# Kernel optimization log

Hardware: AMD Instinct MI355X
Metric: run time of the kernel (lower is better)

Reference implementation:

```python
import jax, jax.numpy as jnp
import numpy as np

DIM = 1024
HEADS = 16
DIM_HEAD = 64
INNER = HEADS * DIM_HEAD  # 1024
EPS = 1e-5


def layer_norm(x, g, b):
    mu = jnp.mean(x, axis=-1, keepdims=True)
    var = jnp.var(x, axis=-1, keepdims=True)
    return (x - mu) * jax.lax.rsqrt(var + EPS) * g + b


def setup_inputs() -> dict:
    key = jax.random.key(0)
    ks = jax.random.split(key, 8)
    s = 0.02
    return {
        "x": jax.random.normal(ks[0], (2, 2048, DIM), dtype=jnp.float32),
        "w_qkv": jax.random.normal(ks[1], (DIM, 3 * INNER), dtype=jnp.float32) * s,
        "w_out": jax.random.normal(ks[2], (INNER, DIM), dtype=jnp.float32) * s,
        "b_out": jnp.zeros((DIM,), jnp.float32),
        "g1": jnp.ones((DIM,), jnp.float32),
        "bt1": jnp.zeros((DIM,), jnp.float32),
        "g2": jnp.ones((DIM,), jnp.float32),
        "bt2": jnp.zeros((DIM,), jnp.float32),
        "w1": jax.random.normal(ks[3], (DIM, DIM), dtype=jnp.float32) * s,  # ff hidden = dim_out = DIM
        "b1": jnp.zeros((DIM,), jnp.float32),
        "w2": jax.random.normal(ks[4], (DIM, DIM), dtype=jnp.float32) * s,
        "b2": jnp.zeros((DIM,), jnp.float32),
    }


def reference(x, w_qkv, w_out, b_out, g1, bt1, g2, bt2, w1, b1, w2, b2):
    b, n, _ = x.shape
    scale = DIM_HEAD ** (-0.5)
    x_in = x
    xl = layer_norm(x, g1, bt1)
    qkv = xl @ w_qkv  # [b, n, 3*inner]
    q, k, v = jnp.split(qkv, 3, axis=-1)
    def split_heads(t):
        return t.reshape(b, n, HEADS, DIM_HEAD).transpose(0, 2, 1, 3)  # b h n d
    q, k, v = map(split_heads, (q, k, v))
    dots = jnp.einsum('bhid,bhjd->bhij', q, k) * scale
    attn = jax.nn.softmax(dots, axis=-1)
    out = jnp.einsum('bhij,bhjd->bhid', attn, v)
    out = out.transpose(0, 2, 1, 3).reshape(b, n, INNER)
    out = out @ w_out + b_out
    out = out + x_in
    h = layer_norm(out, g2, bt2)
    h = jax.nn.gelu(h @ w1 + b1, approximate=False) @ w2 + b2
    return h + out
```

## Files before the change

kernel.cpp:

```cpp
#include <hip/hip_runtime.h>
#include <math.h>

typedef __attribute__((ext_vector_type(4))) float f32x4;
typedef __attribute__((ext_vector_type(8))) short bf16x8;
typedef __attribute__((ext_vector_type(8))) unsigned short u16x8;

#define DIM 1024
#define SEQ 2048
#define NHEADS 16
#define DH 64

__device__ __forceinline__ unsigned short f2bf(float f) {
    unsigned int u = __builtin_bit_cast(unsigned int, f);
    u += 0x7fffu + ((u >> 16) & 1u);
    return (unsigned short)(u >> 16);
}

__device__ __forceinline__ unsigned int cvt_pk_bf16(float lo, float hi) {
    unsigned int r;
    asm("v_cvt_pk_bf16_f32 %0, %1, %2" : "=v"(r) : "v"(lo), "v"(hi));
    return r;
}

__device__ __forceinline__ float fexp2(float x) {
    float r;
    asm("v_exp_f32 %0, %1" : "=v"(r) : "v"(x));
    return r;
}

__device__ __forceinline__ void gld16(const unsigned short* g, unsigned short* l) {
    __builtin_amdgcn_global_load_lds((const __attribute__((address_space(1))) void*)g,
                                     (__attribute__((address_space(3))) void*)l, 16, 0, 0);
}

__global__ __launch_bounds__(256) void wtrans_all(const float* __restrict__ wq,
                                                  const float* __restrict__ wo,
                                                  const float* __restrict__ wf1,
                                                  const float* __restrict__ wf2,
                                                  unsigned short* __restrict__ oq,
                                                  unsigned short* __restrict__ oo,
                                                  unsigned short* __restrict__ of1,
                                                  unsigned short* __restrict__ of2, float sc) {
    int z = blockIdx.z;
    int bxi = blockIdx.x;
    if (z > 0 && bxi >= 32) return;
    const float* w = z == 0 ? wq : z == 1 ? wo : z == 2 ? wf1 : wf2;
    unsigned short* wt = z == 0 ? oq : z == 1 ? oo : z == 2 ? of1 : of2;
    int N = z == 0 ? 3072 : 1024;
    int scale_n = z == 0 ? 1024 : 0;
    const int K = 1024;
    __shared__ float t[32][33];
    int tid = threadIdx.x;
    int n0 = bxi * 32, k0 = blockIdx.y * 32;
    int c = tid & 31, rb = tid >> 5;
#pragma unroll
    for (int i = 0; i < 4; ++i) {
        int r = rb + i * 8;
        t[r][c] = w[(size_t)(k0 + r) * N + n0 + c];
    }
    __syncthreads();
#pragma unroll
    for (int i = 0; i < 4; ++i) {
        int r = rb + i * 8;
        float v = t[c][r];
        if (n0 + r < scale_n) v *= sc;
        wt[(size_t)(n0 + r) * K + k0 + c] = f2bf(v);
    }
}

__global__ __launch_bounds__(256) void ln_kernel(const float* __restrict__ x,
                                                 const float* __restrict__ g,
                                                 const float* __restrict__ bt,
                                                 unsigned short* __restrict__ o) {
    int row = blockIdx.x, tid = threadIdx.x;
    const float4* xr = (const float4*)(x + (size_t)row * DIM);
    float4 v = xr[tid];
    float s1 = v.x + v.y + v.z + v.w;
    float s2 = v.x * v.x + v.y * v.y + v.z * v.z + v.w * v.w;
#pragma unroll
    for (int m = 32; m >= 1; m >>= 1) {
        s1 += __shfl_xor(s1, m);
        s2 += __shfl_xor(s2, m);
    }
    __shared__ float r1[4], r2[4];
    int w = tid >> 6;
    if ((tid & 63) == 0) { r1[w] = s1; r2[w] = s2; }
    __syncthreads();
    s1 = r1[0] + r1[1] + r1[2] + r1[3];
    s2 = r2[0] + r2[1] + r2[2] + r2[3];
    float mu = s1 * (1.0f / DIM);
    float var = s2 * (1.0f / DIM) - mu * mu;
    float rstd = rsqrtf(var + 1e-5f);
    float4 g4 = ((const float4*)g)[tid];
    float4 b4 = ((const float4*)bt)[tid];
    ushort4 ov;
    ov.x = f2bf((v.x - mu) * rstd * g4.x + b4.x);
    ov.y = f2bf((v.y - mu) * rstd * g4.y + b4.y);
    ov.z = f2bf((v.z - mu) * rstd * g4.z + b4.z);
    ov.w = f2bf((v.w - mu) * rstd * g4.w + b4.w);
    *(ushort4*)(o + (size_t)row * DIM + tid * 4) = ov;
}

template <int BN, int BK, int OBF, int BIAS, int GELU_, int RESID>
__global__ __launch_bounds__(256) void gemm_kernel(const unsigned short* __restrict__ A,
                                                   const unsigned short* __restrict__ BT,
                                                   void* __restrict__ C,
                                                   const float* __restrict__ bias,
                                                   const float* __restrict__ resid,
                                                   int M, int N, int K, int nbx) {
    constexpr int U = BK / 8;
    constexpr int NAU = 128 * U;
    constexpr int NBU = BN * U;
    constexpr int PT = (NAU + NBU) / 256;
    constexpr int NJ = BN / 32;
    constexpr int KK = BK / 32;
    __shared__ unsigned short As[3][128 * BK];
    __shared__ unsigned short Bs[3][BN * BK];
    int tid = threadIdx.x;
    int lane = tid & 63, w = tid >> 6;
    int l15 = lane & 15, lhi = lane >> 4;
    int nwg = gridDim.x, wg = blockIdx.x;
    int swz = (wg & 7) * (nwg >> 3) + (wg >> 3);
    int bx = swz % nbx, by = swz / nbx;
    int row0 = by * 128, col0 = bx * BN;
    int wrow = (w >> 1) * 64, wcol = (w & 1) * (16 * NJ);
    f32x4 zero = {0.f, 0.f, 0.f, 0.f};
    f32x4 acc[4][NJ];
#pragma unroll
    for (int i = 0; i < 4; ++i)
#pragma unroll
        for (int j = 0; j < NJ; ++j) acc[i][j] = zero;
    auto stage = [&](int buf, int kt) {
#pragma unroll
        for (int p = 0; p < PT; ++p) {
            if (p * 256 < NAU) {
                int u = tid + p * 256;
                int r = u / U, cu = u % U;
                int scu = cu ^ (r & (U - 1));
                gld16(A + (size_t)(row0 + r) * K + kt * BK + scu * 8, &As[buf][0] + u * 8);
            } else {
                int ub = tid + p * 256 - NAU;
                int r = ub / U, cu = ub % U;
                int scu = cu ^ (r & (U - 1));
                gld16(BT + (size_t)(col0 + r) * K + kt * BK + scu * 8, &Bs[buf][0] + ub * 8);
            }
        }
    };
    int nk = K / BK;
    stage(0, 0);
    stage(1, 1);
    asm volatile("s_waitcnt vmcnt(%0)" ::"i"(PT) : "memory");
    __builtin_amdgcn_s_barrier();
    __builtin_amdgcn_sched_barrier(0);
    int cur = 0;
    for (int kt = 0; kt < nk; ++kt) {
        int nxt2 = cur + 2 >= 3 ? cur - 1 : cur + 2;
        if (kt + 2 < nk) stage(nxt2, kt + 2);
        const unsigned short* Ab = &As[cur][0];
        const unsigned short* Bb = &Bs[cur][0];
        bf16x8 af[4][KK], bfr[NJ][KK];
#pragma unroll
        for (int i = 0; i < 4; ++i)
#pragma unroll
            for (int kk = 0; kk < KK; ++kk) {
                int rr = wrow + i * 16 + l15;
                int up = (kk * 4 + lhi) ^ (rr & (U - 1));
                af[i][kk] = *(const bf16x8*)&Ab[rr * BK + up * 8];
            }
#pragma unroll
        for (int j = 0; j < NJ; ++j)
#pragma unroll
            for (int kk = 0; kk < KK; ++kk) {
                int rr = wcol + j * 16 + l15;
                int up = (kk * 4 + lhi) ^ (rr & (U - 1));
                bfr[j][kk] = *(const bf16x8*)&Bb[rr * BK + up * 8];
            }
#pragma unroll
        for (int kk = 0; kk < KK; ++kk)
#pragma unroll
            for (int i = 0; i < 4; ++i)
#pragma unroll
                for (int j = 0; j < NJ; ++j)
                    acc[i][j] = __builtin_amdgcn_mfma_f32_16x16x32_bf16(af[i][kk], bfr[j][kk],
                                                                        acc[i][j], 0, 0, 0);
        __builtin_amdgcn_sched_barrier(0);
        if (kt + 1 < nk) {
            if (kt + 2 < nk)
                asm volatile("s_waitcnt vmcnt(%0)" ::"i"(PT) : "memory");
            else
                asm volatile("s_waitcnt vmcnt(0)" ::: "memory");
            __builtin_amdgcn_s_barrier();
            __builtin_amdgcn_sched_barrier(0);
        }
        cur = cur + 1 == 3 ? 0 : cur + 1;
    }
#pragma unroll
    for (int i = 0; i < 4; ++i)
#pragma unroll
        for (int j = 0; j < NJ; ++j)
#pragma unroll
            for (int r = 0; r < 4; ++r) {
                int row = row0 + wrow + i * 16 + lhi * 4 + r;
                int col = col0 + wcol + j * 16 + l15;
                float v = acc[i][j][r];
                if (BIAS) v += bias[col];
                if (GELU_) v = 0.5f * v * (1.0f + erff(v * 0.70710678118f));
                if (RESID) v += resid[(size_t)row * N + col];
                if (OBF)
                    ((unsigned short*)C)[(size_t)row * N + col] = f2bf(v);
                else
                    ((float*)C)[(size_t)row * N + col] = v;
            }
}

__global__ __launch_bounds__(256) void vtrans_kernel(const unsigned short* __restrict__ qkv,
                                                     unsigned short* __restrict__ vt) {
    __shared__ unsigned short t[64 * 72];
    int tid = threadIdx.x;
    int nt = blockIdx.x & 31, h = (blockIdx.x >> 5) & 15, b = blockIdx.x >> 9;
#pragma unroll
    for (int p = 0; p < 2; ++p) {
        int c = tid + p * 256;
        int n = c >> 3, s = (c & 7) * 8;
        *(uint4*)&t[n * 72 + s] =
            *(const uint4*)(qkv + (size_t)(b * SEQ + nt * 64 + n) * 3072 + 2048 + h * 64 + s);
    }
    __syncthreads();
#pragma unroll
    for (int p = 0; p < 2; ++p) {
        int c = tid + p * 256;
        int d = c >> 3, s0 = (c & 7) * 8;
        u16x8 val;
#pragma unroll
        for (int j = 0; j < 8; ++j) {
            int s = s0 + j;
            int sig = (s & 32) | ((s & 4) << 2) | ((s & 24) >> 1) | (s & 3);
            val[j] = t[sig * 72 + d];
        }
        *(u16x8*)(vt + ((size_t)(b * NHEADS + h) * DH + d) * SEQ + nt * 64 + s0) = val;
    }
}

__global__ __launch_bounds__(256) void attn_kernel(const unsigned short* __restrict__ qkv,
                                                   const unsigned short* __restrict__ vt,
                                                   unsigned short* __restrict__ o) {
    __shared__ unsigned short Ks[3][64 * 64];
    __shared__ unsigned short Vs[3][64 * 64];
    int tid = threadIdx.x;
    int lane = tid & 63, w = tid >> 6;
    int l15 = lane & 15, lhi = lane >> 4;
    int wg = blockIdx.x;
    int swz = (wg & 7) * 64 + (wg >> 3);
    int qt = swz & 15, h = (swz >> 4) & 15, b = swz >> 8;
    bf16x8 qf[2][2];
#pragma unroll
    for (int qg = 0; qg < 2; ++qg) {
        const unsigned short* qb =
            qkv + (size_t)(b * SEQ + qt * 128 + w * 32 + qg * 16 + l15) * 3072 + h * DH;
        qf[qg][0] = *(const bf16x8*)(qb + lhi * 8);
        qf[qg][1] = *(const bf16x8*)(qb + 32 + lhi * 8);
    }
    f32x4 zero = {0.f, 0.f, 0.f, 0.f};
    f32x4 oacc[2][4], lacc[2];
#pragma unroll
    for (int qg = 0; qg < 2; ++qg) {
        lacc[qg] = zero;
#pragma unroll
        for (int i = 0; i < 4; ++i) oacc[qg][i] = zero;
    }
    const short one_s = (short)0x3F80;
    bf16x8 ones = {one_s, one_s, one_s, one_s, one_s, one_s, one_s, one_s};
    int srow = tid >> 3;
    int scx = (tid & 7) ^ (srow & 7);
    const unsigned short* kb = qkv + (size_t)b * SEQ * 3072 + 1024 + h * DH;
    const unsigned short* vb = vt + (size_t)(b * NHEADS + h) * DH * SEQ;
    const unsigned short* k0 = kb + (size_t)srow * 3072 + scx * 8;
    const unsigned short* v0 = vb + (size_t)srow * SEQ + scx * 8;
    auto stage = [&](int buf, int kt) {
        unsigned short* lk = &Ks[buf][0] + tid * 8;
        unsigned short* lv = &Vs[buf][0] + tid * 8;
        gld16(k0 + (size_t)kt * 64 * 3072, lk);
        gld16(k0 + ((size_t)kt * 64 + 32) * 3072, lk + 2048);
        gld16(v0 + kt * 64, lv);
        gld16(v0 + (size_t)32 * SEQ + kt * 64, lv + 2048);
    };
    const int NT = SEQ / 64;
    stage(0, 0);
    stage(1, 1);
    asm volatile("s_waitcnt vmcnt(4)" ::: "memory");
    __builtin_amdgcn_s_barrier();
    __builtin_amdgcn_sched_barrier(0);
    int kx = l15 & 7;
    int cur = 0;
    for (int kt = 0; kt < NT; ++kt) {
        int nxt2 = cur + 2 >= 3 ? cur - 1 : cur + 2;
        if (kt + 2 < NT) stage(nxt2, kt + 2);
        const unsigned short* Kc = &Ks[cur][0];
        const unsigned short* Vc = &Vs[cur][0];
        f32x4 sacc[2][4];
#pragma unroll
        for (int nt = 0; nt < 4; ++nt) {
            bf16x8 kf0 = *(const bf16x8*)&Kc[(nt * 16 + l15) * 64 + ((lhi ^ kx) * 8)];
            bf16x8 kf1 = *(const bf16x8*)&Kc[(nt * 16 + l15) * 64 + (((4 + lhi) ^ kx) * 8)];
#pragma unroll
            for (int qg = 0; qg < 2; ++qg) {
                f32x4 z = __builtin_amdgcn_mfma_f32_16x16x32_bf16(kf0, qf[qg][0], zero, 0, 0, 0);
                sacc[qg][nt] = __builtin_amdgcn_mfma_f32_16x16x32_bf16(kf1, qf[qg][1], z, 0, 0, 0);
            }
        }
        bf16x8 pf[2][2];
#pragma unroll
        for (int qg = 0; qg < 2; ++qg)
#pragma unroll
            for (int kc = 0; kc < 2; ++kc) {
                union { bf16x8 v; unsigned int u[4]; } pu;
                pu.u[0] = cvt_pk_bf16(fexp2(sacc[qg][2 * kc][0]), fexp2(sacc[qg][2 * kc][1]));
                pu.u[1] = cvt_pk_bf16(fexp2(sacc[qg][2 * kc][2]), fexp2(sacc[qg][2 * kc][3]));
                pu.u[2] = cvt_pk_bf16(fexp2(sacc[qg][2 * kc + 1][0]), fexp2(sacc[qg][2 * kc + 1][1]));
                pu.u[3] = cvt_pk_bf16(fexp2(sacc[qg][2 * kc + 1][2]), fexp2(sacc[qg][2 * kc + 1][3]));
                pf[qg][kc] = pu.v;
            }
#pragma unroll
        for (int dt = 0; dt < 4; ++dt)
#pragma unroll
            for (int kc = 0; kc < 2; ++kc) {
                bf16x8 vf = *(const bf16x8*)&Vc[(dt * 16 + l15) * 64 + (((kc * 4 + lhi) ^ kx) * 8)];
#pragma unroll
                for (int qg = 0; qg < 2; ++qg)
                    oacc[qg][dt] =
                        __builtin_amdgcn_mfma_f32_16x16x32_bf16(vf, pf[qg][kc], oacc[qg][dt], 0, 0, 0);
            }
#pragma unroll
        for (int qg = 0; qg < 2; ++qg) {
            lacc[qg] = __builtin_amdgcn_mfma_f32_16x16x32_bf16(ones, pf[qg][0], lacc[qg], 0, 0, 0);
            lacc[qg] = __builtin_amdgcn_mfma_f32_16x16x32_bf16(ones, pf[qg][1], lacc[qg], 0, 0, 0);
        }
        __builtin_amdgcn_sched_barrier(0);
        if (kt + 1 < NT) {
            if (kt + 2 < NT)
                asm volatile("s_waitcnt vmcnt(4)" ::: "memory");
            else
                asm volatile("s_waitcnt vmcnt(0)" ::: "memory");
            __builtin_amdgcn_s_barrier();
            __builtin_amdgcn_sched_barrier(0);
        }
        cur = cur + 1 == 3 ? 0 : cur + 1;
    }
#pragma unroll
    for (int qg = 0; qg < 2; ++qg) {
        float rl = 1.0f / lacc[qg][0];
        size_t orow = (size_t)(b * SEQ + qt * 128 + w * 32 + qg * 16 + l15) * DIM + h * DH;
#pragma unroll
        for (int dt = 0; dt < 4; ++dt) {
            ushort4 st;
            st.x = f2bf(oacc[qg][dt][0] * rl);
            st.y = f2bf(oacc[qg][dt][1] * rl);
            st.z = f2bf(oacc[qg][dt][2] * rl);
            st.w = f2bf(oacc[qg][dt][3] * rl);
            *(ushort4*)(o + orow + dt * 16 + lhi * 4) = st;
        }
    }
}

extern "C" void kernel_launch(void* const* d_in, const int* in_sizes, int n_in,
                              void* d_out, int out_size, void* d_ws, size_t ws_size,
                              hipStream_t stream) {
    (void)in_sizes; (void)n_in; (void)out_size; (void)ws_size;
    const float* x = (const float*)d_in[0];
    const float* w_qkv = (const float*)d_in[1];
    const float* w_out = (const float*)d_in[2];
    const float* b_out = (const float*)d_in[3];
    const float* g1 = (const float*)d_in[4];
    const float* bt1 = (const float*)d_in[5];
    const float* g2 = (const float*)d_in[6];
    const float* bt2 = (const float*)d_in[7];
    const float* w1 = (const float*)d_in[8];
    const float* b1 = (const float*)d_in[9];
    const float* w2 = (const float*)d_in[10];
    const float* b2 = (const float*)d_in[11];
    float* out = (float*)d_out;

    char* ws = (char*)d_ws;
    size_t off = 0;
    auto alloc = [&](size_t bytes) {
        void* p = ws + off;
        off += (bytes + 255) & ~(size_t)255;
        return p;
    };
    const int R = 2 * SEQ;
    unsigned short* xl    = (unsigned short*)alloc((size_t)R * DIM * 2);
    unsigned short* wqkvT = (unsigned short*)alloc((size_t)3 * DIM * DIM * 2);
    unsigned short* woutT = (unsigned short*)alloc((size_t)DIM * DIM * 2);
    unsigned short* w1T   = (unsigned short*)alloc((size_t)DIM * DIM * 2);
    unsigned short* w2T   = (unsigned short*)alloc((size_t)DIM * DIM * 2);
    unsigned short* qkvb  = (unsigned short*)alloc((size_t)R * 3 * DIM * 2);
    unsigned short* vtb   = (unsigned short*)alloc((size_t)R * DIM * 2);
    unsigned short* attO  = (unsigned short*)alloc((size_t)R * DIM * 2);
    unsigned short* h2    = (unsigned short*)alloc((size_t)R * DIM * 2);
    unsigned short* ffn1  = (unsigned short*)alloc((size_t)R * DIM * 2);

    const float CS = 0.125f * 1.44269504f;
    wtrans_all<<<dim3(96, 32, 4), 256, 0, stream>>>(w_qkv, w_out, w1, w2, wqkvT, woutT, w1T, w2T, CS);

    ln_kernel<<<R, 256, 0, stream>>>(x, g1, bt1, xl);
    gemm_kernel<128, 32, 1, 0, 0, 0><<<dim3((3 * DIM / 128) * (R / 128)), 256, 0, stream>>>(
        xl, wqkvT, qkvb, nullptr, nullptr, R, 3 * DIM, DIM, 3 * DIM / 128);
    vtrans_kernel<<<2 * NHEADS * (SEQ / 64), 256, 0, stream>>>(qkvb, vtb);
    attn_kernel<<<2 * NHEADS * (SEQ / 128), 256, 0, stream>>>(qkvb, vtb, attO);
    gemm_kernel<64, 64, 0, 1, 0, 1><<<dim3((DIM / 64) * (R / 128)), 256, 0, stream>>>(
        attO, woutT, out, b_out, x, R, DIM, DIM, DIM / 64);
    ln_kernel<<<R, 256, 0, stream>>>(out, g2, bt2, h2);
    gemm_kernel<64, 64, 1, 1, 1, 0><<<dim3((DIM / 64) * (R / 128)), 256, 0, stream>>>(
        h2, w1T, ffn1, b1, nullptr, R, DIM, DIM, DIM / 64);
    gemm_kernel<64, 64, 0, 1, 0, 1><<<dim3((DIM / 64) * (R / 128)), 256, 0, stream>>>(
        ffn1, w2T, out, b2, out, R, DIM, DIM, DIM / 64);
}
```

Before: 170.0 us.

## Split attention over two key halves with a separate combine kernel

Splits each attention workgroup's key range into two halves, doubling the grid to 1024 blocks. Each block writes unnormalised partial outputs (bf16) and row sums, and a new combine kernel adds the halves and normalises. The triple-buffered async K/V pipeline is replaced with a single buffer that waits for each load before computing, which removes load/compute overlap. It also adds extra global traffic and a kernel launch, and rounds partial sums to bf16 before they are combined. The combine is valid because the softmax uses no running max, so the partial sums are plain sums.

```diff
diff --git a/kernel.cpp b/kernel.cpp
--- a/kernel.cpp
+++ b/kernel.cpp
@@ -14,6 +14,11 @@
     unsigned int u = __builtin_bit_cast(unsigned int, f);
     u += 0x7fffu + ((u >> 16) & 1u);
     return (unsigned short)(u >> 16);
+}
+
+__device__ __forceinline__ float bf2f(unsigned short s) {
+    unsigned int u = (unsigned int)s << 16;
+    return __builtin_bit_cast(float, u);
 }
 
 __device__ __forceinline__ unsigned int cvt_pk_bf16(float lo, float hi) {
@@ -243,15 +248,16 @@
 
 __global__ __launch_bounds__(256) void attn_kernel(const unsigned short* __restrict__ qkv,
                                                    const unsigned short* __restrict__ vt,
-                                                   unsigned short* __restrict__ o) {
-    __shared__ unsigned short Ks[3][64 * 64];
-    __shared__ unsigned short Vs[3][64 * 64];
+                                                   unsigned short* __restrict__ po,
+                                                   float* __restrict__ pl) {
+    __shared__ unsigned short Ks[64 * 64];
+    __shared__ unsigned short Vs[64 * 64];
     int tid = threadIdx.x;
     int lane = tid & 63, w = tid >> 6;
     int l15 = lane & 15, lhi = lane >> 4;
     int wg = blockIdx.x;
-    int swz = (wg & 7) * 64 + (wg >> 3);
-    int qt = swz & 15, h = (swz >> 4) & 15, b = swz >> 8;
+    int swz = (wg & 7) * 128 + (wg >> 3);
+    int qt = swz & 15, half = (swz >> 4) & 1, h = (swz >> 5) & 15, b = swz >> 9;
     bf16x8 qf[2][2];
 #pragma unroll
     for (int qg = 0; qg < 2; ++qg) {
@@ -276,32 +282,26 @@
     const unsigned short* vb = vt + (size_t)(b * NHEADS + h) * DH * SEQ;
     const unsigned short* k0 = kb + (size_t)srow * 3072 + scx * 8;
     const unsigned short* v0 = vb + (size_t)srow * SEQ + scx * 8;
-    auto stage = [&](int buf, int kt) {
-        unsigned short* lk = &Ks[buf][0] + tid * 8;
-        unsigned short* lv = &Vs[buf][0] + tid * 8;
-        gld16(k0 + (size_t)kt * 64 * 3072, lk);
-        gld16(k0 + ((size_t)kt * 64 + 32) * 3072, lk + 2048);
-        gld16(v0 + kt * 64, lv);
-        gld16(v0 + (size_t)32 * SEQ + kt * 64, lv + 2048);
+    auto stage = [&](int kg) {
+        unsigned short* lk = &Ks[0] + tid * 8;
+        unsigned short* lv = &Vs[0] + tid * 8;
+        gld16(k0 + (size_t)kg * 64 * 3072, lk);
+        gld16(k0 + ((size_t)kg * 64 + 32) * 3072, lk + 2048);
+        gld16(v0 + kg * 64, lv);
+        gld16(v0 + (size_t)32 * SEQ + kg * 64, lv + 2048);
     };
-    const int NT = SEQ / 64;
-    stage(0, 0);
-    stage(1, 1);
-    asm volatile("s_waitcnt vmcnt(4)" ::: "memory");
-    __builtin_amdgcn_s_barrier();
-    __builtin_amdgcn_sched_barrier(0);
     int kx = l15 & 7;
-    int cur = 0;
-    for (int kt = 0; kt < NT; ++kt) {
-        int nxt2 = cur + 2 >= 3 ? cur - 1 : cur + 2;
-        if (kt + 2 < NT) stage(nxt2, kt + 2);
-        const unsigned short* Kc = &Ks[cur][0];
-        const unsigned short* Vc = &Vs[cur][0];
+    const int NT2 = SEQ / 64 / 2;
+    for (int kt = 0; kt < NT2; ++kt) {
+        stage(half * NT2 + kt);
+        asm volatile("s_waitcnt vmcnt(0)" ::: "memory");
+        __builtin_amdgcn_s_barrier();
+        __builtin_amdgcn_sched_barrier(0);
         f32x4 sacc[2][4];
 #pragma unroll
         for (int nt = 0; nt < 4; ++nt) {
-            bf16x8 kf0 = *(const bf16x8*)&Kc[(nt * 16 + l15) * 64 + ((lhi ^ kx) * 8)];
-            bf16x8 kf1 = *(const bf16x8*)&Kc[(nt * 16 + l15) * 64 + (((4 + lhi) ^ kx) * 8)];
+            bf16x8 kf0 = *(const bf16x8*)&Ks[(nt * 16 + l15) * 64 + ((lhi ^ kx) * 8)];
+            bf16x8 kf1 = *(const bf16x8*)&Ks[(nt * 16 + l15) * 64 + (((4 + lhi) ^ kx) * 8)];
 #pragma unroll
             for (int qg = 0; qg < 2; ++qg) {
                 f32x4 z = __builtin_amdgcn_mfma_f32_16x16x32_bf16(kf0, qf[qg][0], zero, 0, 0, 0);
@@ -324,7 +324,7 @@
         for (int dt = 0; dt < 4; ++dt)
 #pragma unroll
             for (int kc = 0; kc < 2; ++kc) {
-                bf16x8 vf = *(const bf16x8*)&Vc[(dt * 16 + l15) * 64 + (((kc * 4 + lhi) ^ kx) * 8)];
+                bf16x8 vf = *(const bf16x8*)&Vs[(dt * 16 + l15) * 64 + (((kc * 4 + lhi) ^ kx) * 8)];
 #pragma unroll
                 for (int qg = 0; qg < 2; ++qg)
                     oacc[qg][dt] =
@@ -336,30 +336,42 @@
             lacc[qg] = __builtin_amdgcn_mfma_f32_16x16x32_bf16(ones, pf[qg][1], lacc[qg], 0, 0, 0);
         }
         __builtin_amdgcn_sched_barrier(0);
-        if (kt + 1 < NT) {
-            if (kt + 2 < NT)
-                asm volatile("s_waitcnt vmcnt(4)" ::: "memory");
-            else
-                asm volatile("s_waitcnt vmcnt(0)" ::: "memory");
+        if (kt + 1 < NT2) {
             __builtin_amdgcn_s_barrier();
             __builtin_amdgcn_sched_barrier(0);
         }
-        cur = cur + 1 == 3 ? 0 : cur + 1;
     }
 #pragma unroll
     for (int qg = 0; qg < 2; ++qg) {
-        float rl = 1.0f / lacc[qg][0];
-        size_t orow = (size_t)(b * SEQ + qt * 128 + w * 32 + qg * 16 + l15) * DIM + h * DH;
+        int rrow = b * SEQ + qt * 128 + w * 32 + qg * 16 + l15;
+        unsigned short* pob = po + ((size_t)half * 4096 + rrow) * DIM + h * DH;
 #pragma unroll
         for (int dt = 0; dt < 4; ++dt) {
             ushort4 st;
-            st.x = f2bf(oacc[qg][dt][0] * rl);
-            st.y = f2bf(oacc[qg][dt][1] * rl);
-            st.z = f2bf(oacc[qg][dt][2] * rl);
-            st.w = f2bf(oacc[qg][dt][3] * rl);
-            *(ushort4*)(o + orow + dt * 16 + lhi * 4) = st;
-        }
-    }
+            st.x = f2bf(oacc[qg][dt][0]);
+            st.y = f2bf(oacc[qg][dt][1]);
+            st.z = f2bf(oacc[qg][dt][2]);
+            st.w = f2bf(oacc[qg][dt][3]);
+            *(ushort4*)(pob + dt * 16 + lhi * 4) = st;
+        }
+        if (lhi == 0) pl[((size_t)half * 4096 + rrow) * NHEADS + h] = lacc[qg][0];
+    }
+}
+
+__global__ __launch_bounds__(256) void attn_combine(const unsigned short* __restrict__ po,
+                                                    const float* __restrict__ pl,
+                                                    unsigned short* __restrict__ o) {
+    int r = blockIdx.x, tid = threadIdx.x;
+    int d0 = tid * 4, h = d0 >> 6;
+    ushort4 a = *(const ushort4*)(po + (size_t)r * DIM + d0);
+    ushort4 c = *(const ushort4*)(po + (size_t)(4096 + r) * DIM + d0);
+    float rl = 1.0f / (pl[(size_t)r * NHEADS + h] + pl[(size_t)(4096 + r) * NHEADS + h]);
+    ushort4 ov;
+    ov.x = f2bf((bf2f(a.x) + bf2f(c.x)) * rl);
+    ov.y = f2bf((bf2f(a.y) + bf2f(c.y)) * rl);
+    ov.z = f2bf((bf2f(a.z) + bf2f(c.z)) * rl);
+    ov.w = f2bf((bf2f(a.w) + bf2f(c.w)) * rl);
+    *(ushort4*)(o + (size_t)r * DIM + d0) = ov;
 }
 
 extern "C" void kernel_launch(void* const* d_in, const int* in_sizes, int n_in,
@@ -398,6 +410,8 @@
     unsigned short* attO  = (unsigned short*)alloc((size_t)R * DIM * 2);
     unsigned short* h2    = (unsigned short*)alloc((size_t)R * DIM * 2);
     unsigned short* ffn1  = (unsigned short*)alloc((size_t)R * DIM * 2);
+    unsigned short* po = (unsigned short*)alloc((size_t)2 * R * DIM * 2);
+    float* pl = (float*)alloc((size_t)2 * R * NHEADS * 4);
 
     const float CS = 0.125f * 1.44269504f;
     wtrans_all<<<dim3(96, 32, 4), 256, 0, stream>>>(w_qkv, w_out, w1, w2, wqkvT, woutT, w1T, w2T, CS);
@@ -406,7 +420,8 @@
     gemm_kernel<128, 32, 1, 0, 0, 0><<<dim3((3 * DIM / 128) * (R / 128)), 256, 0, stream>>>(
         xl, wqkvT, qkvb, nullptr, nullptr, R, 3 * DIM, DIM, 3 * DIM / 128);
     vtrans_kernel<<<2 * NHEADS * (SEQ / 64), 256, 0, stream>>>(qkvb, vtb);
-    attn_kernel<<<2 * NHEADS * (SEQ / 128), 256, 0, stream>>>(qkvb, vtb, attO);
+    attn_kernel<<<2 * NHEADS * (SEQ / 128) * 2, 256, 0, stream>>>(qkvb, vtb, po, pl);
+    attn_combine<<<R, 256, 0, stream>>>(po, pl, attO);
     gemm_kernel<64, 64, 0, 1, 0, 1><<<dim3((DIM / 64) * (R / 128)), 256, 0, stream>>>(
         attO, woutT, out, b_out, x, R, DIM, DIM, DIM / 64);
     ln_kernel<<<R, 256, 0, stream>>>(out, g2, bt2, h2);
```

Result: no change. 173.1 us (+1.8%).
